# Kernel tuning notes

Hardware: AMD Instinct MI355X
Metric: run time of the kernel (lower is better)

The kernel has to match this reference:

```python
import jax, jax.numpy as jnp
import numpy as np

N_GROUP = 8
TOPK_GROUP = 4
TOP_K = 8
ROUTED_SCALING_FACTOR = 2.5


def setup_inputs() -> dict:
    key = jax.random.key(0)
    ks = jax.random.split(key, 6)
    T, H, I, E = 256, 1024, 512, 32
    x = jax.random.normal(ks[0], (T, H), dtype=jnp.float32)
    gate_w = jax.random.normal(ks[1], (H, E), dtype=jnp.float32) * 0.05
    e_score_bias = jax.random.normal(ks[2], (E,), dtype=jnp.float32) * 0.05
    Wg = jax.random.normal(ks[3], (E, H, I), dtype=jnp.float32) * 0.02
    Wu = jax.random.normal(ks[4], (E, H, I), dtype=jnp.float32) * 0.02
    Wd = jax.random.normal(ks[5], (E, I, H), dtype=jnp.float32) * 0.02
    return {"x": x, "gate_w": gate_w, "e_score_bias": e_score_bias,
            "Wg": Wg, "Wu": Wu, "Wd": Wd}


def _route_ds3(x, gate_w, e_score_bias):
    # DeepSeek-V3 group-limited top-k routing (routing_ds3 in source).
    T = x.shape[0]
    E = gate_w.shape[1]
    logits = x @ gate_w                      # [T, E]
    scores = jax.nn.sigmoid(logits)
    scores_for_choice = scores + e_score_bias[None, :]
    gsz = E // N_GROUP
    grouped = scores_for_choice.reshape(T, N_GROUP, gsz)
    # group score = sum of top-2 expert scores in group
    group_scores = jnp.sum(jax.lax.top_k(grouped, 2)[0], axis=-1)     # [T, n_group]
    _, group_idx = jax.lax.top_k(group_scores, TOPK_GROUP)            # [T, topk_group]
    rows = jnp.arange(T)[:, None]
    group_mask = jnp.zeros((T, N_GROUP), scores.dtype).at[rows, group_idx].set(1.0)
    score_mask = jnp.repeat(group_mask, gsz, axis=-1)                 # [T, E]
    masked = jnp.where(score_mask > 0, scores_for_choice, 0.0)
    _, topk_idx = jax.lax.top_k(masked, TOP_K)                        # [T, k]
    topk_w = jnp.take_along_axis(scores, topk_idx, axis=1)            # gather raw scores
    topk_w = topk_w / (jnp.sum(topk_w, axis=-1, keepdims=True) + 1e-20)
    topk_w = topk_w * ROUTED_SCALING_FACTOR
    return topk_idx, topk_w


def reference(x, gate_w, e_score_bias, Wg, Wu, Wd):
    T = x.shape[0]
    E = gate_w.shape[1]
    topk_idx, topk_w = _route_ds3(x, gate_w, e_score_bias)
    # dense [T, E] routing-weight matrix (topk indices are unique per row)
    rows = jnp.arange(T)[:, None]
    rw = jnp.zeros((T, E), x.dtype).at[rows, topk_idx].set(topk_w)
    # expert gated MLP (silu), combined with routing weights
    g = jnp.einsum('th,ehi->tei', x, Wg)      # [T, E, I]
    u = jnp.einsum('th,ehi->tei', x, Wu)
    a = jax.nn.silu(g) * u
    y = jnp.einsum('tei,eih->teh', a, Wd)     # [T, E, H]
    out = jnp.einsum('te,teh->th', rw, y)     # weighted combine
    return out
```

## Files before the change

kernel.cpp:

```cpp
#include <hip/hip_runtime.h>
#include <cstdint>
#include <cmath>

constexpr int TT   = 256;
constexpr int HD   = 1024;
constexpr int IDIM = 512;
constexpr int NE   = 32;
constexpr int NGRP = 8;
constexpr int TKG  = 4;
constexpr int TOPK = 8;
constexpr float RSCALE = 2.5f;

constexpr int NSX  = HD / 32;
constexpr int NSA  = IDIM / 32;
constexpr int SLAB = 16 * 64 * 8;

typedef float    f32x4 __attribute__((ext_vector_type(4)));
typedef _Float16 half8 __attribute__((ext_vector_type(8)));

constexpr size_t WS_CNT   = 0;
constexpr size_t WS_TOK   = 256;
constexpr size_t WS_WL    = WS_TOK   + (size_t)NE * TT * 4;
constexpr size_t WS_TSLOT = WS_WL    + (size_t)NE * TT * 4;
constexpr size_t WS_OFFS  = WS_TSLOT + (size_t)TT * TOPK * 4;
constexpr size_t WS_XE    = WS_OFFS  + 256;
constexpr size_t WS_A     = WS_XE + (size_t)NE * NSX * SLAB * 2;

#define GLOAD16(GP, LP) __builtin_amdgcn_global_load_lds(                      \
    (const __attribute__((address_space(1))) unsigned int*)(GP),               \
    (__attribute__((address_space(3))) unsigned int*)(LP), 16, 0, 0)

#define WAITVM(N) asm volatile("s_waitcnt vmcnt(" #N ")" ::: "memory")

__global__ __launch_bounds__(256) void k_route(
    const float* __restrict__ x, const float* __restrict__ gw,
    const float* __restrict__ bias, int* __restrict__ cnt,
    int* __restrict__ tok, float* __restrict__ wl, int* __restrict__ tslot)
{
    int t = blockIdx.x;
    int tid = threadIdx.x;
    int e2 = (tid & 15) * 2;
    int c  = tid >> 4;
    const float* xr = x + (size_t)t * HD;

    float a0 = 0.f, a1 = 0.f;
    int h0 = c * (HD / 16);
#pragma unroll 8
    for (int h = h0; h < h0 + HD / 16; ++h) {
        float xv = xr[h];
        float2 wv = *(const float2*)&gw[(size_t)h * NE + e2];
        a0 += xv * wv.x;
        a1 += xv * wv.y;
    }

    __shared__ float part[16][NE];
    part[c][e2]     = a0;
    part[c][e2 + 1] = a1;
    __syncthreads();

    __shared__ float sc[NE], sfc[NE];
    if (tid < NE) {
        float s = 0.f;
#pragma unroll
        for (int cc = 0; cc < 16; ++cc) s += part[cc][tid];
        float sig = 1.f / (1.f + expf(-s));
        sc[tid]  = sig;
        sfc[tid] = sig + bias[tid];
    }
    __syncthreads();

    if (tid == 0) {
        float gs[NGRP];
        for (int g = 0; g < NGRP; ++g) {
            float m1 = -3.0e38f, m2 = -3.0e38f;
            for (int j = 0; j < 4; ++j) {
                float v = sfc[4 * g + j];
                if (v > m1) { m2 = m1; m1 = v; } else if (v > m2) m2 = v;
            }
            gs[g] = m1 + m2;
        }
        bool gsel[NGRP];
        for (int g = 0; g < NGRP; ++g) gsel[g] = false;
        for (int r = 0; r < TKG; ++r) {
            int bi = -1; float bv = -3.0e38f;
            for (int g = 0; g < NGRP; ++g)
                if (!gsel[g] && gs[g] > bv) { bv = gs[g]; bi = g; }
            gsel[bi] = true;
        }
        float masked[NE];
        for (int i = 0; i < NE; ++i) masked[i] = gsel[i >> 2] ? sfc[i] : 0.0f;
        int   idx[TOPK]; float wv[TOPK]; float wsum = 0.f;
        for (int r = 0; r < TOPK; ++r) {
            int bi = -1; float bv = -3.0e38f;
            for (int i = 0; i < NE; ++i)
                if (masked[i] > bv) { bv = masked[i]; bi = i; }
            masked[bi] = -3.0e38f;
            idx[r] = bi; wv[r] = sc[bi]; wsum += wv[r];
        }
        float inv = RSCALE / (wsum + 1e-20f);
        for (int r = 0; r < TOPK; ++r) {
            int ee = idx[r];
            int pos = atomicAdd(&cnt[ee], 1);
            tok[(size_t)ee * TT + pos] = t;
            wl [(size_t)ee * TT + pos] = wv[r] * inv;
            tslot[t * TOPK + r] = ee * TT + pos;
        }
    }
}

__global__ __launch_bounds__(256) void k_pack(
    const float* __restrict__ x, const int* __restrict__ cnt,
    const int* __restrict__ tok, _Float16* __restrict__ Xe,
    int* __restrict__ offs)
{
    int bid  = blockIdx.x;
    int tid  = threadIdx.x;
    if (bid == 0 && tid == 0) {
        int s = 0;
        for (int e = 0; e < NE; ++e) { offs[e] = s; s += cnt[e]; }
    }
    int xcd  = bid & 7;
    int slot = bid >> 3;
    int e    = xcd * 4 + (slot & 3);
    int s    = slot >> 2;
    int n_e = cnt[e];
    if (n_e == 0) return;
    int w = tid >> 6, lane = tid & 63;
    int m16 = lane & 15, q = lane >> 4;
    _Float16* base = Xe + ((size_t)e * NSX + s) * SLAB;
#pragma unroll
    for (int k = 0; k < 4; ++k) {
        int mt = w + k * 4;
        int slot2 = mt * 16 + m16;
        if (slot2 >= n_e) slot2 = n_e - 1;
        int t = tok[e * TT + slot2];
        const float* src = x + (size_t)t * HD + s * 32 + q * 8;
        f32x4 v0 = *(const f32x4*)src;
        f32x4 v1 = *(const f32x4*)(src + 4);
        half8 h;
        h[0] = (_Float16)v0.x; h[1] = (_Float16)v0.y; h[2] = (_Float16)v0.z; h[3] = (_Float16)v0.w;
        h[4] = (_Float16)v1.x; h[5] = (_Float16)v1.y; h[6] = (_Float16)v1.z; h[7] = (_Float16)v1.w;
        *(half8*)(base + ((size_t)mt * 64 + lane) * 8) = h;
    }
}

__global__ __launch_bounds__(128, 1) void k_gateup(
    const _Float16* __restrict__ Xe, const float* __restrict__ Wg,
    const float* __restrict__ Wu, const int* __restrict__ cnt,
    _Float16* __restrict__ A)
{
    int bid  = blockIdx.x;
    int xcd  = bid & 7;
    int slot = bid >> 3;
    int e    = xcd * 4 + (slot & 3);
    int rest = slot >> 2;
    int ig    = rest & 31;
    int ttile = rest >> 5;
    int n_e = cnt[e];
    if (ttile * 128 >= n_e) return;
    int mtbase = ttile * 8;
    int i0 = ig * 16;
    int tid  = threadIdx.x;
    int w    = tid >> 6;
    int lane = tid & 63;
    int m16 = lane & 15, q = lane >> 4;

    __shared__ __align__(16) float    LG[3][32][16];
    __shared__ __align__(16) float    LU[3][32][16];
    __shared__ __align__(16) _Float16 LA[3][4096];

    const _Float16* aslab = Xe + (size_t)e * NSX * SLAB + (size_t)mtbase * 512;
    const float* gw0 = Wg + (size_t)e * HD * IDIM + i0;
    const float* uw0 = Wu + (size_t)e * HD * IDIM + i0;

    f32x4 accG[4], accU[4];
#pragma unroll
    for (int mt = 0; mt < 4; ++mt) {
        accG[mt] = (f32x4){0.f, 0.f, 0.f, 0.f};
        accU[mt] = (f32x4){0.f, 0.f, 0.f, 0.f};
    }

#define GU_STAGE(B, KS)                                                        \
    { const float* wp_ = (w == 0) ? gw0 : uw0;                                 \
      float* lp_ = (w == 0) ? &LG[B][0][0] : &LU[B][0][0];                     \
      _Pragma("unroll")                                                        \
      for (int i_ = 0; i_ < 2; ++i_) {                                         \
        int row_  = i_ * 16 + (lane >> 2);                                     \
        int csrc_ = ((lane & 3) << 2) ^ (((row_ >> 3) & 3) << 2);              \
        GLOAD16(wp_ + ((size_t)(KS) * 32 + row_) * IDIM + csrc_,               \
                lp_ + i_ * 256);                                               \
      }                                                                        \
      _Pragma("unroll")                                                        \
      for (int i_ = 0; i_ < 4; ++i_) {                                         \
        int off_ = (w * 4 + i_) * 512;                                         \
        GLOAD16(aslab + (size_t)(KS) * SLAB + off_ + lane * 8, &LA[B][off_]);  \
      } }

#define GU_COMPUTE(B)                                                          \
    { int lc = m16 ^ (q << 2);                                                 \
      half8 bg, bu;                                                            \
      _Pragma("unroll")                                                        \
      for (int j_ = 0; j_ < 8; ++j_) {                                         \
        bg[j_] = (_Float16)LG[B][q * 8 + j_][lc];                              \
        bu[j_] = (_Float16)LU[B][q * 8 + j_][lc];                              \
      }                                                                        \
      __builtin_amdgcn_s_setprio(1);                                           \
      _Pragma("unroll")                                                        \
      for (int mt_ = 0; mt_ < 4; ++mt_) {                                      \
        half8 afr = *(const half8*)&LA[B][(w * 4 + mt_) * 512 + lane * 8];     \
        accG[mt_] = __builtin_amdgcn_mfma_f32_16x16x32_f16(afr, bg, accG[mt_], 0, 0, 0); \
        accU[mt_] = __builtin_amdgcn_mfma_f32_16x16x32_f16(afr, bu, accU[mt_], 0, 0, 0); \
      }                                                                        \
      __builtin_amdgcn_s_setprio(0); }

    constexpr int NK = HD / 32;
    GU_STAGE(0, 0) GU_STAGE(1, 1)

#pragma unroll
    for (int ks = 0; ks < NK; ++ks) {
        __builtin_amdgcn_s_barrier();
        if (ks + 2 < NK) GU_STAGE((ks + 2) % 3, ks + 2)
        if      (ks + 2 < NK)  { WAITVM(12); }
        else if (ks + 1 < NK)  { WAITVM(6);  }
        else                   { WAITVM(0);  }
        __builtin_amdgcn_s_barrier();
        __builtin_amdgcn_sched_barrier(0);
        GU_COMPUTE(ks % 3)
    }
#undef GU_STAGE
#undef GU_COMPUTE

    int iyw = ig;
    _Float16* aout = A + ((size_t)e * NSA + (iyw >> 1)) * SLAB;
    int cj   = m16 & 7;
    int lsub = ((iyw * 2 + (m16 >> 3)) & 3) * 16;
#pragma unroll
    for (int mt = 0; mt < 4; ++mt) {
#pragma unroll
        for (int r = 0; r < 4; ++r) {
            float g = accG[mt][r], u = accU[mt][r];
            float a = (g / (1.f + expf(-g))) * u;
            int lp = (q * 4 + r) + lsub;
            aout[((size_t)(mtbase + w * 4 + mt) * 64 + lp) * 8 + cj] = (_Float16)a;
        }
    }
}

__global__ __launch_bounds__(128, 1) void k_down(
    const _Float16* __restrict__ A, const float* __restrict__ Wd,
    const int* __restrict__ cnt, const int* __restrict__ offs,
    const float* __restrict__ wl, float* __restrict__ Y)
{
    int bid  = blockIdx.x;
    int xcd  = bid & 7;
    int slot = bid >> 3;
    int e    = xcd * 4 + (slot & 3);
    int rest = slot >> 2;
    int hg    = rest & 63;
    int ttile = rest >> 6;
    int n_e = cnt[e];
    if (ttile * 128 >= n_e) return;
    int mtbase = ttile * 8;
    int h0 = hg * 16;
    int tid  = threadIdx.x;
    int w    = tid >> 6;
    int lane = tid & 63;
    int m16 = lane & 15, q = lane >> 4;

    __shared__ __align__(16) float    LD[3][32][16];
    __shared__ __align__(16) _Float16 LA[3][4096];

    const _Float16* aslab = A + (size_t)e * NSA * SLAB + (size_t)mtbase * 512;
    const float* dw0 = Wd + (size_t)e * IDIM * HD + h0;

    f32x4 acc[4];
#pragma unroll
    for (int mt = 0; mt < 4; ++mt) acc[mt] = (f32x4){0.f, 0.f, 0.f, 0.f};

#define DN_STAGE(B, KS)                                                        \
    { int row_  = w * 16 + (lane >> 2);                                        \
      int csrc_ = ((lane & 3) << 2) ^ (((row_ >> 3) & 3) << 2);                \
      GLOAD16(dw0 + ((size_t)(KS) * 32 + row_) * HD + csrc_,                   \
              &LD[B][w * 16][0]);                                              \
      _Pragma("unroll")                                                        \
      for (int i_ = 0; i_ < 4; ++i_) {                                         \
        int off_ = (w * 4 + i_) * 512;                                         \
        GLOAD16(aslab + (size_t)(KS) * SLAB + off_ + lane * 8, &LA[B][off_]);  \
      } }

#define DN_COMPUTE(B)                                                          \
    { int lc = m16 ^ (q << 2);                                                 \
      half8 bd;                                                                \
      _Pragma("unroll")                                                        \
      for (int j_ = 0; j_ < 8; ++j_) bd[j_] = (_Float16)LD[B][q * 8 + j_][lc]; \
      __builtin_amdgcn_s_setprio(1);                                           \
      _Pragma("unroll")                                                        \
      for (int mt_ = 0; mt_ < 4; ++mt_) {                                      \
        half8 afr = *(const half8*)&LA[B][(w * 4 + mt_) * 512 + lane * 8];     \
        acc[mt_] = __builtin_amdgcn_mfma_f32_16x16x32_f16(afr, bd, acc[mt_], 0, 0, 0); \
      }                                                                        \
      __builtin_amdgcn_s_setprio(0); }

    constexpr int NK = IDIM / 32;
    DN_STAGE(0, 0) DN_STAGE(1, 1)

#pragma unroll
    for (int ks = 0; ks < NK; ++ks) {
        __builtin_amdgcn_s_barrier();
        if (ks + 2 < NK) DN_STAGE((ks + 2) % 3, ks + 2)
        if      (ks + 2 < NK)  { WAITVM(10); }
        else if (ks + 1 < NK)  { WAITVM(5);  }
        else                   { WAITVM(0);  }
        __builtin_amdgcn_s_barrier();
        __builtin_amdgcn_sched_barrier(0);
        DN_COMPUTE(ks % 3)
    }
#undef DN_STAGE
#undef DN_COMPUTE

    int oe = offs[e];
    int col = h0 + m16;
#pragma unroll
    for (int mt = 0; mt < 4; ++mt) {
#pragma unroll
        for (int r = 0; r < 4; ++r) {
            int slot2 = ttile * 128 + (w * 4 + mt) * 16 + q * 4 + r;
            if (slot2 < n_e) {
                float wt = wl[(size_t)e * TT + slot2];
                Y[(size_t)(oe + slot2) * HD + col] = wt * acc[mt][r];
            }
        }
    }
}

__global__ __launch_bounds__(256) void k_combine(
    const float* __restrict__ Y, const int* __restrict__ tslot,
    const int* __restrict__ offs, float* __restrict__ out)
{
    int t = blockIdx.x, tid = threadIdx.x;
    f32x4 s = (f32x4){0.f, 0.f, 0.f, 0.f};
#pragma unroll
    for (int r = 0; r < TOPK; ++r) {
        int ts  = tslot[t * TOPK + r];
        int e   = ts >> 8;
        int pos = ts & 255;
        const float* yp = Y + (size_t)(offs[e] + pos) * HD + tid * 4;
        f32x4 v = *(const f32x4*)yp;
        s.x += v.x; s.y += v.y; s.z += v.z; s.w += v.w;
    }
    *(f32x4*)&out[(size_t)t * HD + tid * 4] = s;
}

extern "C" void kernel_launch(void* const* d_in, const int* in_sizes, int n_in,
                              void* d_out, int out_size, void* d_ws, size_t ws_size,
                              hipStream_t stream) {
    const float* x    = (const float*)d_in[0];
    const float* gw   = (const float*)d_in[1];
    const float* bias = (const float*)d_in[2];
    const float* Wg   = (const float*)d_in[3];
    const float* Wu   = (const float*)d_in[4];
    const float* Wd   = (const float*)d_in[5];
    float* out = (float*)d_out;

    char* ws = (char*)d_ws;
    int*      cnt   = (int*)(ws + WS_CNT);
    int*      tok   = (int*)(ws + WS_TOK);
    float*    wl    = (float*)(ws + WS_WL);
    int*      tslot = (int*)(ws + WS_TSLOT);
    int*      offs  = (int*)(ws + WS_OFFS);
    _Float16* Xe    = (_Float16*)(ws + WS_XE);
    _Float16* A     = (_Float16*)(ws + WS_A);
    float*    Y     = (float*)(ws + WS_XE);

    hipMemsetAsync(ws, 0, 256, stream);

    k_route<<<TT, 256, 0, stream>>>(x, gw, bias, cnt, tok, wl, tslot);
    k_pack<<<NE * NSX, 256, 0, stream>>>(x, cnt, tok, Xe, offs);
    k_gateup<<<NE * 2 * (IDIM / 16), 128, 0, stream>>>(Xe, Wg, Wu, cnt, A);
    k_down<<<NE * 2 * (HD / 16), 128, 0, stream>>>(A, Wd, cnt, offs, wl, Y);
    k_combine<<<TT, 256, 0, stream>>>(Y, tslot, offs, out);
}
```

Baseline: 267.0 us.

## Widen expert GEMM tiles to 512-thread blocks with 4-stage pipeline

```diff
diff --git a/kernel.cpp b/kernel.cpp
--- a/kernel.cpp
+++ b/kernel.cpp
@@ -144,7 +144,7 @@
     }
 }
 
-__global__ __launch_bounds__(128, 1) void k_gateup(
+__global__ __launch_bounds__(512, 1) void k_gateup(
     const _Float16* __restrict__ Xe, const float* __restrict__ Wg,
     const float* __restrict__ Wu, const int* __restrict__ cnt,
     _Float16* __restrict__ A)
@@ -154,99 +154,104 @@
     int slot = bid >> 3;
     int e    = xcd * 4 + (slot & 3);
     int rest = slot >> 2;
-    int ig    = rest & 31;
-    int ttile = rest >> 5;
+    int ig   = rest & 7;
+    int tt   = rest >> 3;
     int n_e = cnt[e];
-    if (ttile * 128 >= n_e) return;
-    int mtbase = ttile * 8;
-    int i0 = ig * 16;
+    if (tt * 128 >= n_e) return;
+    int mtbase = tt * 8;
     int tid  = threadIdx.x;
     int w    = tid >> 6;
     int lane = tid & 63;
     int m16 = lane & 15, q = lane >> 4;
-
-    __shared__ __align__(16) float    LG[3][32][16];
-    __shared__ __align__(16) float    LU[3][32][16];
-    __shared__ __align__(16) _Float16 LA[3][4096];
-
-    const _Float16* aslab = Xe + (size_t)e * NSX * SLAB + (size_t)mtbase * 512;
-    const float* gw0 = Wg + (size_t)e * HD * IDIM + i0;
-    const float* uw0 = Wu + (size_t)e * HD * IDIM + i0;
-
-    f32x4 accG[4], accU[4];
-#pragma unroll
-    for (int mt = 0; mt < 4; ++mt) {
-        accG[mt] = (f32x4){0.f, 0.f, 0.f, 0.f};
-        accU[mt] = (f32x4){0.f, 0.f, 0.f, 0.f};
-    }
+    int wr = w & 3, wc = w >> 2;
+
+    __shared__ __align__(16) float    LG[4][32][64];
+    __shared__ __align__(16) float    LU[4][32][64];
+    __shared__ __align__(16) _Float16 LA[4][4096];
+
+    const _Float16* asrc = Xe + (size_t)e * NSX * SLAB + (size_t)(mtbase + w) * 512 + lane * 8;
+    const float* gp = Wg + (size_t)e * HD * IDIM + ig * 64;
+    const float* up = Wu + (size_t)e * HD * IDIM + ig * 64;
+    int wrow  = 4 * w + (lane >> 4);
+    int wcsrc = ((lane & 15) << 2) ^ (((w >> 1) & 1) << 4);
+
+    f32x4 accG[2][2], accU[2][2];
+#pragma unroll
+    for (int a_ = 0; a_ < 2; ++a_)
+#pragma unroll
+        for (int b_ = 0; b_ < 2; ++b_) {
+            accG[a_][b_] = (f32x4){0.f, 0.f, 0.f, 0.f};
+            accU[a_][b_] = (f32x4){0.f, 0.f, 0.f, 0.f};
+        }
 
 #define GU_STAGE(B, KS)                                                        \
-    { const float* wp_ = (w == 0) ? gw0 : uw0;                                 \
-      float* lp_ = (w == 0) ? &LG[B][0][0] : &LU[B][0][0];                     \
-      _Pragma("unroll")                                                        \
-      for (int i_ = 0; i_ < 2; ++i_) {                                         \
-        int row_  = i_ * 16 + (lane >> 2);                                     \
-        int csrc_ = ((lane & 3) << 2) ^ (((row_ >> 3) & 3) << 2);              \
-        GLOAD16(wp_ + ((size_t)(KS) * 32 + row_) * IDIM + csrc_,               \
-                lp_ + i_ * 256);                                               \
-      }                                                                        \
-      _Pragma("unroll")                                                        \
-      for (int i_ = 0; i_ < 4; ++i_) {                                         \
-        int off_ = (w * 4 + i_) * 512;                                         \
-        GLOAD16(aslab + (size_t)(KS) * SLAB + off_ + lane * 8, &LA[B][off_]);  \
-      } }
+    { GLOAD16(asrc + (size_t)(KS) * SLAB, &LA[B][w * 512]);                    \
+      GLOAD16(gp + ((size_t)(KS) * 32 + wrow) * IDIM + wcsrc, &LG[B][4 * w][0]); \
+      GLOAD16(up + ((size_t)(KS) * 32 + wrow) * IDIM + wcsrc, &LU[B][4 * w][0]); }
 
 #define GU_COMPUTE(B)                                                          \
-    { int lc = m16 ^ (q << 2);                                                 \
-      half8 bg, bu;                                                            \
+    { int c0 = wc * 32 + (m16 ^ ((q & 1) << 4));                               \
+      int c1 = wc * 32 + ((16 + m16) ^ ((q & 1) << 4));                        \
+      half8 bg0, bg1, bu0, bu1;                                                \
       _Pragma("unroll")                                                        \
       for (int j_ = 0; j_ < 8; ++j_) {                                         \
-        bg[j_] = (_Float16)LG[B][q * 8 + j_][lc];                              \
-        bu[j_] = (_Float16)LU[B][q * 8 + j_][lc];                              \
+        bg0[j_] = (_Float16)LG[B][q * 8 + j_][c0];                             \
+        bg1[j_] = (_Float16)LG[B][q * 8 + j_][c1];                             \
+        bu0[j_] = (_Float16)LU[B][q * 8 + j_][c0];                             \
+        bu1[j_] = (_Float16)LU[B][q * 8 + j_][c1];                             \
       }                                                                        \
+      half8 a0 = *(const half8*)&LA[B][wr * 512 + lane * 8];                   \
+      half8 a1 = *(const half8*)&LA[B][(wr + 4) * 512 + lane * 8];             \
       __builtin_amdgcn_s_setprio(1);                                           \
-      _Pragma("unroll")                                                        \
-      for (int mt_ = 0; mt_ < 4; ++mt_) {                                      \
-        half8 afr = *(const half8*)&LA[B][(w * 4 + mt_) * 512 + lane * 8];     \
-        accG[mt_] = __builtin_amdgcn_mfma_f32_16x16x32_f16(afr, bg, accG[mt_], 0, 0, 0); \
-        accU[mt_] = __builtin_amdgcn_mfma_f32_16x16x32_f16(afr, bu, accU[mt_], 0, 0, 0); \
-      }                                                                        \
+      accG[0][0] = __builtin_amdgcn_mfma_f32_16x16x32_f16(a0, bg0, accG[0][0], 0, 0, 0); \
+      accG[0][1] = __builtin_amdgcn_mfma_f32_16x16x32_f16(a0, bg1, accG[0][1], 0, 0, 0); \
+      accU[0][0] = __builtin_amdgcn_mfma_f32_16x16x32_f16(a0, bu0, accU[0][0], 0, 0, 0); \
+      accU[0][1] = __builtin_amdgcn_mfma_f32_16x16x32_f16(a0, bu1, accU[0][1], 0, 0, 0); \
+      accG[1][0] = __builtin_amdgcn_mfma_f32_16x16x32_f16(a1, bg0, accG[1][0], 0, 0, 0); \
+      accG[1][1] = __builtin_amdgcn_mfma_f32_16x16x32_f16(a1, bg1, accG[1][1], 0, 0, 0); \
+      accU[1][0] = __builtin_amdgcn_mfma_f32_16x16x32_f16(a1, bu0, accU[1][0], 0, 0, 0); \
+      accU[1][1] = __builtin_amdgcn_mfma_f32_16x16x32_f16(a1, bu1, accU[1][1], 0, 0, 0); \
       __builtin_amdgcn_s_setprio(0); }
 
     constexpr int NK = HD / 32;
-    GU_STAGE(0, 0) GU_STAGE(1, 1)
+    GU_STAGE(0, 0) GU_STAGE(1, 1) GU_STAGE(2, 2)
 
 #pragma unroll
     for (int ks = 0; ks < NK; ++ks) {
         __builtin_amdgcn_s_barrier();
-        if (ks + 2 < NK) GU_STAGE((ks + 2) % 3, ks + 2)
-        if      (ks + 2 < NK)  { WAITVM(12); }
-        else if (ks + 1 < NK)  { WAITVM(6);  }
-        else                   { WAITVM(0);  }
+        if (ks + 3 < NK) GU_STAGE((ks + 3) & 3, ks + 3)
+        if      (ks + 4 <= NK) { WAITVM(9); }
+        else if (ks + 3 == NK) { WAITVM(6); }
+        else if (ks + 2 == NK) { WAITVM(3); }
+        else                   { WAITVM(0); }
         __builtin_amdgcn_s_barrier();
         __builtin_amdgcn_sched_barrier(0);
-        GU_COMPUTE(ks % 3)
+        GU_COMPUTE(ks & 3)
     }
 #undef GU_STAGE
 #undef GU_COMPUTE
 
-    int iyw = ig;
-    _Float16* aout = A + ((size_t)e * NSA + (iyw >> 1)) * SLAB;
-    int cj   = m16 & 7;
-    int lsub = ((iyw * 2 + (m16 >> 3)) & 3) * 16;
-#pragma unroll
-    for (int mt = 0; mt < 4; ++mt) {
-#pragma unroll
-        for (int r = 0; r < 4; ++r) {
-            float g = accG[mt][r], u = accU[mt][r];
-            float a = (g / (1.f + expf(-g))) * u;
-            int lp = (q * 4 + r) + lsub;
-            aout[((size_t)(mtbase + w * 4 + mt) * 64 + lp) * 8 + cj] = (_Float16)a;
-        }
-    }
-}
-
-__global__ __launch_bounds__(128, 1) void k_down(
+    int sa = ig * 2 + wc;
+    _Float16* aout = A + ((size_t)e * NSA + sa) * SLAB;
+    int jp = m16 & 7;
+#pragma unroll
+    for (int mtl = 0; mtl < 2; ++mtl) {
+        int mtg = mtbase + wr + 4 * mtl;
+#pragma unroll
+        for (int cg = 0; cg < 2; ++cg) {
+            int qp = cg * 2 + (m16 >> 3);
+#pragma unroll
+            for (int r = 0; r < 4; ++r) {
+                float g = accG[mtl][cg][r], u = accU[mtl][cg][r];
+                float a = (g / (1.f + expf(-g))) * u;
+                int lanep = qp * 16 + q * 4 + r;
+                aout[((size_t)mtg * 64 + lanep) * 8 + jp] = (_Float16)a;
+            }
+        }
+    }
+}
+
+__global__ __launch_bounds__(512, 1) void k_down(
     const _Float16* __restrict__ A, const float* __restrict__ Wd,
     const int* __restrict__ cnt, const int* __restrict__ offs,
     const float* __restrict__ wl, float* __restrict__ Y)
@@ -256,78 +261,89 @@
     int slot = bid >> 3;
     int e    = xcd * 4 + (slot & 3);
     int rest = slot >> 2;
-    int hg    = rest & 63;
-    int ttile = rest >> 6;
+    int hg   = rest & 7;
+    int tt   = rest >> 3;
     int n_e = cnt[e];
-    if (ttile * 128 >= n_e) return;
-    int mtbase = ttile * 8;
-    int h0 = hg * 16;
+    if (tt * 128 >= n_e) return;
+    int mtbase = tt * 8;
+    int h0 = hg * 128;
     int tid  = threadIdx.x;
     int w    = tid >> 6;
     int lane = tid & 63;
     int m16 = lane & 15, q = lane >> 4;
-
-    __shared__ __align__(16) float    LD[3][32][16];
-    __shared__ __align__(16) _Float16 LA[3][4096];
-
-    const _Float16* aslab = A + (size_t)e * NSA * SLAB + (size_t)mtbase * 512;
-    const float* dw0 = Wd + (size_t)e * IDIM * HD + h0;
-
-    f32x4 acc[4];
-#pragma unroll
-    for (int mt = 0; mt < 4; ++mt) acc[mt] = (f32x4){0.f, 0.f, 0.f, 0.f};
+    int wr = w & 3, wc = w >> 2;
+
+    __shared__ __align__(16) float    LD[4][32][128];
+    __shared__ __align__(16) _Float16 LA[4][4096];
+
+    const _Float16* asrc = A + (size_t)e * NSA * SLAB + (size_t)(mtbase + w) * 512 + lane * 8;
+    const float* dp = Wd + (size_t)e * IDIM * HD + h0;
+    int rA = 2 * w + (lane >> 5);
+    int rB = 2 * (w + 8) + (lane >> 5);
+    int csA = ((lane & 31) << 2) ^ (((w >> 2) & 1) << 4);
+    int csB = ((lane & 31) << 2) ^ ((((w + 8) >> 2) & 1) << 4);
+
+    f32x4 acc[2][4];
+#pragma unroll
+    for (int a_ = 0; a_ < 2; ++a_)
+#pragma unroll
+        for (int b_ = 0; b_ < 4; ++b_) acc[a_][b_] = (f32x4){0.f, 0.f, 0.f, 0.f};
 
 #define DN_STAGE(B, KS)                                                        \
-    { int row_  = w * 16 + (lane >> 2);                                        \
-      int csrc_ = ((lane & 3) << 2) ^ (((row_ >> 3) & 3) << 2);                \
-      GLOAD16(dw0 + ((size_t)(KS) * 32 + row_) * HD + csrc_,                   \
-              &LD[B][w * 16][0]);                                              \
+    { GLOAD16(asrc + (size_t)(KS) * SLAB, &LA[B][w * 512]);                    \
+      GLOAD16(dp + ((size_t)(KS) * 32 + rA) * HD + csA, &LD[B][2 * w][0]);     \
+      GLOAD16(dp + ((size_t)(KS) * 32 + rB) * HD + csB, &LD[B][2 * (w + 8)][0]); }
+
+#define DN_COMPUTE(B)                                                          \
+    { half8 bd[4];                                                             \
       _Pragma("unroll")                                                        \
-      for (int i_ = 0; i_ < 4; ++i_) {                                         \
-        int off_ = (w * 4 + i_) * 512;                                         \
-        GLOAD16(aslab + (size_t)(KS) * SLAB + off_ + lane * 8, &LA[B][off_]);  \
-      } }
-
-#define DN_COMPUTE(B)                                                          \
-    { int lc = m16 ^ (q << 2);                                                 \
-      half8 bd;                                                                \
-      _Pragma("unroll")                                                        \
-      for (int j_ = 0; j_ < 8; ++j_) bd[j_] = (_Float16)LD[B][q * 8 + j_][lc]; \
+      for (int cg = 0; cg < 4; ++cg) {                                         \
+        int col = (wc * 2 + (cg >> 1)) * 32 + ((((cg & 1) << 4) + m16) ^ ((q & 1) << 4)); \
+        _Pragma("unroll")                                                      \
+        for (int j_ = 0; j_ < 8; ++j_) bd[cg][j_] = (_Float16)LD[B][q * 8 + j_][col]; \
+      }                                                                        \
+      half8 a0 = *(const half8*)&LA[B][wr * 512 + lane * 8];                   \
+      half8 a1 = *(const half8*)&LA[B][(wr + 4) * 512 + lane * 8];             \
       __builtin_amdgcn_s_setprio(1);                                           \
       _Pragma("unroll")                                                        \
-      for (int mt_ = 0; mt_ < 4; ++mt_) {                                      \
-        half8 afr = *(const half8*)&LA[B][(w * 4 + mt_) * 512 + lane * 8];     \
-        acc[mt_] = __builtin_amdgcn_mfma_f32_16x16x32_f16(afr, bd, acc[mt_], 0, 0, 0); \
+      for (int cg = 0; cg < 4; ++cg) {                                         \
+        acc[0][cg] = __builtin_amdgcn_mfma_f32_16x16x32_f16(a0, bd[cg], acc[0][cg], 0, 0, 0); \
+        acc[1][cg] = __builtin_amdgcn_mfma_f32_16x16x32_f16(a1, bd[cg], acc[1][cg], 0, 0, 0); \
       }                                                                        \
       __builtin_amdgcn_s_setprio(0); }
 
     constexpr int NK = IDIM / 32;
-    DN_STAGE(0, 0) DN_STAGE(1, 1)
+    DN_STAGE(0, 0) DN_STAGE(1, 1) DN_STAGE(2, 2)
 
 #pragma unroll
     for (int ks = 0; ks < NK; ++ks) {
         __builtin_amdgcn_s_barrier();
-        if (ks + 2 < NK) DN_STAGE((ks + 2) % 3, ks + 2)
-        if      (ks + 2 < NK)  { WAITVM(10); }
-        else if (ks + 1 < NK)  { WAITVM(5);  }
-        else                   { WAITVM(0);  }
+        if (ks + 3 < NK) DN_STAGE((ks + 3) & 3, ks + 3)
+        if      (ks + 4 <= NK) { WAITVM(9); }
+        else if (ks + 3 == NK) { WAITVM(6); }
+        else if (ks + 2 == NK) { WAITVM(3); }
+        else                   { WAITVM(0); }
         __builtin_amdgcn_s_barrier();
         __builtin_amdgcn_sched_barrier(0);
-        DN_COMPUTE(ks % 3)
+        DN_COMPUTE(ks & 3)
     }
 #undef DN_STAGE
 #undef DN_COMPUTE
 
     int oe = offs[e];
-    int col = h0 + m16;
-#pragma unroll
-    for (int mt = 0; mt < 4; ++mt) {
-#pragma unroll
-        for (int r = 0; r < 4; ++r) {
-            int slot2 = ttile * 128 + (w * 4 + mt) * 16 + q * 4 + r;
-            if (slot2 < n_e) {
-                float wt = wl[(size_t)e * TT + slot2];
-                Y[(size_t)(oe + slot2) * HD + col] = wt * acc[mt][r];
+#pragma unroll
+    for (int mtl = 0; mtl < 2; ++mtl) {
+        int mtg = wr + 4 * mtl;
+#pragma unroll
+        for (int cg = 0; cg < 4; ++cg) {
+            int col = h0 + wc * 64 + cg * 16 + m16;
+#pragma unroll
+            for (int r = 0; r < 4; ++r) {
+                int slot2 = tt * 128 + mtg * 16 + q * 4 + r;
+                if (slot2 < n_e) {
+                    float wt = wl[(size_t)e * TT + slot2];
+                    Y[(size_t)(oe + slot2) * HD + col] = wt * acc[mtl][cg][r];
+                }
             }
         }
     }
@@ -376,7 +392,7 @@
 
     k_route<<<TT, 256, 0, stream>>>(x, gw, bias, cnt, tok, wl, tslot);
     k_pack<<<NE * NSX, 256, 0, stream>>>(x, cnt, tok, Xe, offs);
-    k_gateup<<<NE * 2 * (IDIM / 16), 128, 0, stream>>>(Xe, Wg, Wu, cnt, A);
-    k_down<<<NE * 2 * (HD / 16), 128, 0, stream>>>(A, Wd, cnt, offs, wl, Y);
+    k_gateup<<<512, 512, 0, stream>>>(Xe, Wg, Wu, cnt, A);
+    k_down<<<512, 512, 0, stream>>>(A, Wd, cnt, offs, wl, Y);
     k_combine<<<TT, 256, 0, stream>>>(Y, tslot, offs, out);
 }
```

Result: faster. 246.3 us (-7.8%).
